# Optimization experiments

Hardware: AMD Instinct MI355X
Metric: run time of the kernel (lower is better)

Reference implementation:

```python
import jax, jax.numpy as jnp
import numpy as np

B, W, DIN, DOUT, H = 256, 20, 1024, 1024, 1280
EPS = 1e-5
SLOPE = 0.01  # torch LeakyReLU default negative_slope


def setup_inputs() -> dict:
    key = jax.random.key(0)
    ks = jax.random.split(key, 16)
    s = lambda fan_in: 1.0 / np.sqrt(fan_in)
    return {
        'embs': jax.random.normal(ks[0], (B, W, DIN), jnp.float32),
        'W1': jax.random.uniform(ks[1], (W, DIN, H), jnp.float32, -s(DIN), s(DIN)),
        'b1': jax.random.uniform(ks[2], (W, H), jnp.float32, -s(DIN), s(DIN)),
        'g1': jnp.ones((W, H), jnp.float32), 'bn1': jnp.zeros((W, H), jnp.float32),
        'W2': jax.random.uniform(ks[3], (W, H, H), jnp.float32, -s(H), s(H)),
        'b2': jax.random.uniform(ks[4], (W, H), jnp.float32, -s(H), s(H)),
        'g2': jnp.ones((W, H), jnp.float32), 'bn2': jnp.zeros((W, H), jnp.float32),
        'W3': jax.random.uniform(ks[5], (W, H, H), jnp.float32, -s(H), s(H)),
        'b3': jax.random.uniform(ks[6], (W, H), jnp.float32, -s(H), s(H)),
        'g3': jnp.ones((W, H), jnp.float32), 'bn3': jnp.zeros((W, H), jnp.float32),
        'W4': jax.random.uniform(ks[7], (W, H, DOUT), jnp.float32, -s(H), s(H)),
        'b4': jax.random.uniform(ks[8], (W, DOUT), jnp.float32, -s(H), s(H)),
    }


def _layernorm(x, g, b):
    # x: [B, W, H]; g, b: [W, H] (per-word affine params)
    mu = jnp.mean(x, axis=-1, keepdims=True)
    var = jnp.mean(jnp.square(x - mu), axis=-1, keepdims=True)
    return (x - mu) * jax.lax.rsqrt(var + EPS) * g + b


def _leaky_relu(x):
    return jnp.where(x >= 0, x, SLOPE * x)


def reference(embs, W1, b1, g1, bn1, W2, b2, g2, bn2, W3, b3, g3, bn3, W4, b4):
    # Stacked per-word towers: equivalent to the torch per-word Python loop.
    # embs: [B, W, DIN] -> out: [B, W, DOUT]
    h = jnp.einsum('bwi,wih->bwh', embs, W1) + b1
    h = _leaky_relu(_layernorm(h, g1, bn1))
    h = jnp.einsum('bwh,whk->bwk', h, W2) + b2
    h = _leaky_relu(_layernorm(h, g2, bn2))
    h = jnp.einsum('bwh,whk->bwk', h, W3) + b3
    h = _leaky_relu(_layernorm(h, g3, bn3))
    out = jnp.einsum('bwh,who->bwo', h, W4) + b4
    return out
```

## Files before the change

kernel.cpp:

```cpp
#include <hip/hip_runtime.h>
#include <hip/hip_bf16.h>


typedef unsigned short u16;
typedef __attribute__((ext_vector_type(8))) short bf16x8;
typedef __attribute__((ext_vector_type(4))) float f32x4;

constexpr int CB = 256;
constexpr int CW = 20;
constexpr int CDIN = 1024;
constexpr int CDOUT = 1024;
constexpr int CH = 1280;
constexpr float CEPS = 1e-5f;
constexpr float CSLOPE = 0.01f;

__device__ __forceinline__ u16 f2bf(float f) {
    union { float f; unsigned u; } v; v.f = f;
    unsigned r = v.u + 0x7fffu + ((v.u >> 16) & 1u);
    return (u16)(r >> 16);
}
__device__ __forceinline__ unsigned pk2(float a, float b) {
    return (unsigned)f2bf(a) | ((unsigned)f2bf(b) << 16);
}

template <int K, int N, bool AF32>
__global__ __launch_bounds__(256, 6) void gemm_kernel(
    const void* __restrict__ Aptr, const float* __restrict__ Bw,
    const float* __restrict__ bias, float* __restrict__ Out)
{
    constexpr int NB  = N / 64;
    constexpr int NK  = K / 32;
    constexpr int NWG = 4 * NB * CW;
    constexpr int CPX = NWG / 8;

    __shared__ u16 As[2][64 * 40];
    __shared__ u16 Bs[2][64 * 40];

    const int t   = threadIdx.x;
    const int bid = blockIdx.x;
    const int logical = (bid & 7) * CPX + (bid >> 3);
    const int mb = logical & 3;
    const int nb = (logical >> 2) % NB;
    const int w  = logical / (4 * NB);

    const int m0g = mb * 64;
    const int n0g = nb * 64;

    const int lane = t & 63;
    const int wid  = t >> 6;
    const int m0 = (wid >> 1) * 32;
    const int n0 = (wid & 1) * 32;
    const int lrow = lane & 15;
    const int kg   = lane >> 4;

    const int ar = t >> 2;
    const int ac = (t & 3) * 8;
    const u16*   agp  = (const u16*)Aptr   + ((size_t)(m0g + ar) * CW + w) * K + ac;
    const float* agpf = (const float*)Aptr + ((size_t)(m0g + ar) * CW + w) * K + ac;

    const int bn = t & 63;
    const int bq = t >> 6;
    const float* bgp = Bw + (size_t)w * K * N + (size_t)bq * 8 * N + (n0g + bn);

    f32x4 acc[2][2];
    #pragma unroll
    for (int i = 0; i < 2; ++i)
        #pragma unroll
        for (int j = 0; j < 2; ++j)
            acc[i][j] = (f32x4){0.f, 0.f, 0.f, 0.f};

    uint4 a0;
    float4 af0, af1;
    float bstg[8];

    auto loadA = [&](int k0) {
        if constexpr (AF32) {
            const float4* p = reinterpret_cast<const float4*>(agpf + k0);
            af0 = p[0]; af1 = p[1];
        } else {
            a0 = *reinterpret_cast<const uint4*>(agp + k0);
        }
    };
    auto loadB = [&](int k0) {
        const float* p = bgp + (size_t)k0 * N;
        #pragma unroll
        for (int i = 0; i < 8; ++i) bstg[i] = p[(size_t)i * N];
    };
    auto writeA = [&](int buf) {
        if constexpr (AF32) {
            uint4 pk;
            pk.x = pk2(af0.x, af0.y); pk.y = pk2(af0.z, af0.w);
            pk.z = pk2(af1.x, af1.y); pk.w = pk2(af1.z, af1.w);
            *reinterpret_cast<uint4*>(&As[buf][ar * 40 + ac]) = pk;
        } else {
            *reinterpret_cast<uint4*>(&As[buf][ar * 40 + ac]) = a0;
        }
    };
    auto writeB = [&](int buf) {
        uint4 pk;
        pk.x = pk2(bstg[0], bstg[1]); pk.y = pk2(bstg[2], bstg[3]);
        pk.z = pk2(bstg[4], bstg[5]); pk.w = pk2(bstg[6], bstg[7]);
        *reinterpret_cast<uint4*>(&Bs[buf][bn * 40 + bq * 8]) = pk;
    };
    auto compute = [&](int buf) {
        bf16x8 af[2], bfr[2];
        #pragma unroll
        for (int i = 0; i < 2; ++i)
            af[i] = *reinterpret_cast<const bf16x8*>(
                &As[buf][(m0 + i * 16 + lrow) * 40 + kg * 8]);
        #pragma unroll
        for (int j = 0; j < 2; ++j)
            bfr[j] = *reinterpret_cast<const bf16x8*>(
                &Bs[buf][(n0 + j * 16 + lrow) * 40 + kg * 8]);
        #pragma unroll
        for (int i = 0; i < 2; ++i)
            #pragma unroll
            for (int j = 0; j < 2; ++j)
                acc[i][j] = __builtin_amdgcn_mfma_f32_16x16x32_bf16(
                    af[i], bfr[j], acc[i][j], 0, 0, 0);
    };

    loadA(0); loadB(0);
    writeA(0); writeB(0);
    __syncthreads();

    int buf = 0;
    for (int ks = 0; ks < NK; ++ks) {
        if (ks + 1 < NK) { loadA((ks + 1) * 32); loadB((ks + 1) * 32); }
        compute(buf);
        if (ks + 1 < NK) { writeA(buf ^ 1); writeB(buf ^ 1); }
        __syncthreads();
        buf ^= 1;
    }

    const int rb = (lane >> 4) * 4;
    #pragma unroll
    for (int j = 0; j < 2; ++j) {
        const int gn = n0g + n0 + j * 16 + lrow;
        const float bv = bias[(size_t)w * N + gn];
        #pragma unroll
        for (int i = 0; i < 2; ++i) {
            const int gm = m0g + m0 + i * 16 + rb;
            #pragma unroll
            for (int r = 0; r < 4; ++r) {
                Out[((size_t)(gm + r) * CW + w) * N + gn] = acc[i][j][r] + bv;
            }
        }
    }
}

__global__ __launch_bounds__(320) void ln_lrelu_kernel(
    const float* __restrict__ h, const float* __restrict__ g,
    const float* __restrict__ bta, u16* __restrict__ out)
{
    const int row = blockIdx.x;
    const int w = row % CW;
    const int t = threadIdx.x;

    const float4 v = reinterpret_cast<const float4*>(h + (size_t)row * CH)[t];
    float s  = v.x + v.y + v.z + v.w;
    float sq = v.x * v.x + v.y * v.y + v.z * v.z + v.w * v.w;
    #pragma unroll
    for (int o = 32; o > 0; o >>= 1) {
        s  += __shfl_down(s, o, 64);
        sq += __shfl_down(sq, o, 64);
    }
    __shared__ float ss[5], sg[5];
    const int lane = t & 63, wv = t >> 6;
    if (lane == 0) { ss[wv] = s; sg[wv] = sq; }
    __syncthreads();
    float S = 0.f, Q = 0.f;
    #pragma unroll
    for (int i = 0; i < 5; ++i) { S += ss[i]; Q += sg[i]; }
    const float mean = S * (1.0f / CH);
    const float var  = Q * (1.0f / CH) - mean * mean;
    const float rstd = rsqrtf(var + CEPS);

    const float4 gg = reinterpret_cast<const float4*>(g   + (size_t)w * CH)[t];
    const float4 bb = reinterpret_cast<const float4*>(bta + (size_t)w * CH)[t];
    float4 y;
    y.x = (v.x - mean) * rstd * gg.x + bb.x;
    y.y = (v.y - mean) * rstd * gg.y + bb.y;
    y.z = (v.z - mean) * rstd * gg.z + bb.z;
    y.w = (v.w - mean) * rstd * gg.w + bb.w;
    y.x = y.x >= 0.f ? y.x : CSLOPE * y.x;
    y.y = y.y >= 0.f ? y.y : CSLOPE * y.y;
    y.z = y.z >= 0.f ? y.z : CSLOPE * y.z;
    y.w = y.w >= 0.f ? y.w : CSLOPE * y.w;
    ushort4 o4;
    o4.x = f2bf(y.x); o4.y = f2bf(y.y); o4.z = f2bf(y.z); o4.w = f2bf(y.w);
    reinterpret_cast<ushort4*>(out + (size_t)row * CH)[t] = o4;
}

extern "C" void kernel_launch(void* const* d_in, const int* in_sizes, int n_in,
                              void* d_out, int out_size, void* d_ws, size_t ws_size,
                              hipStream_t stream)
{
    const float* embs = (const float*)d_in[0];
    const float* W1  = (const float*)d_in[1];
    const float* b1  = (const float*)d_in[2];
    const float* g1  = (const float*)d_in[3];
    const float* bn1 = (const float*)d_in[4];
    const float* W2  = (const float*)d_in[5];
    const float* b2  = (const float*)d_in[6];
    const float* g2  = (const float*)d_in[7];
    const float* bn2 = (const float*)d_in[8];
    const float* W3  = (const float*)d_in[9];
    const float* b3  = (const float*)d_in[10];
    const float* g3  = (const float*)d_in[11];
    const float* bn3 = (const float*)d_in[12];
    const float* W4  = (const float*)d_in[13];
    const float* b4  = (const float*)d_in[14];

    char* ws = (char*)d_ws;
    float* h_raw = (float*)ws;
    u16*   a_bf  = (u16*)(ws + 26214400);

    gemm_kernel<CDIN, CH, true><<<4 * (CH / 64) * CW, 256, 0, stream>>>(embs, W1, b1, h_raw);
    ln_lrelu_kernel<<<CB * CW, 320, 0, stream>>>(h_raw, g1, bn1, a_bf);
    gemm_kernel<CH, CH, false><<<4 * (CH / 64) * CW, 256, 0, stream>>>(a_bf, W2, b2, h_raw);
    ln_lrelu_kernel<<<CB * CW, 320, 0, stream>>>(h_raw, g2, bn2, a_bf);
    gemm_kernel<CH, CH, false><<<4 * (CH / 64) * CW, 256, 0, stream>>>(a_bf, W3, b3, h_raw);
    ln_lrelu_kernel<<<CB * CW, 320, 0, stream>>>(h_raw, g3, bn3, a_bf);
    gemm_kernel<CH, CDOUT, false><<<4 * (CDOUT / 64) * CW, 256, 0, stream>>>(a_bf, W4, b4, (float*)d_out);
}
```

Measured before the change: 334.9 us.

## Double K tile to 64 with two-stage register prefetch in GEMM

The GEMM K step grows from 32 to 64 and global loads are prefetched two tiles ahead into two register staging slots. The loop is unrolled by two over the LDS double buffers. The fp32-to-bf16 packing now uses the HIP packed conversion intrinsic, and the occupancy hint drops to 4 to make room for the extra registers. This halves the number of barriers and hides more global latency, at the cost of more VGPRs and LDS per block and possibly lower occupancy.

Result: slower. 638.6 us (+90.7%).

```diff
diff --git a/kernel.cpp b/kernel.cpp
--- a/kernel.cpp
+++ b/kernel.cpp
@@ -20,21 +20,23 @@
     return (u16)(r >> 16);
 }
 __device__ __forceinline__ unsigned pk2(float a, float b) {
-    return (unsigned)f2bf(a) | ((unsigned)f2bf(b) << 16);
+    __hip_bfloat162 h = __float22bfloat162_rn(float2{a, b});
+    union { __hip_bfloat162 h; unsigned u; } v; v.h = h;
+    return v.u;
 }
 
 template <int K, int N, bool AF32>
-__global__ __launch_bounds__(256, 6) void gemm_kernel(
+__global__ __launch_bounds__(256, 4) void gemm_kernel(
     const void* __restrict__ Aptr, const float* __restrict__ Bw,
     const float* __restrict__ bias, float* __restrict__ Out)
 {
     constexpr int NB  = N / 64;
-    constexpr int NK  = K / 32;
+    constexpr int NK  = K / 64;
     constexpr int NWG = 4 * NB * CW;
     constexpr int CPX = NWG / 8;
 
-    __shared__ u16 As[2][64 * 40];
-    __shared__ u16 Bs[2][64 * 40];
+    __shared__ u16 As[2][64 * 72];
+    __shared__ u16 Bs[2][64 * 72];
 
     const int t   = threadIdx.x;
     const int bid = blockIdx.x;
@@ -54,13 +56,13 @@
     const int kg   = lane >> 4;
 
     const int ar = t >> 2;
-    const int ac = (t & 3) * 8;
+    const int ac = (t & 3) * 16;
     const u16*   agp  = (const u16*)Aptr   + ((size_t)(m0g + ar) * CW + w) * K + ac;
     const float* agpf = (const float*)Aptr + ((size_t)(m0g + ar) * CW + w) * K + ac;
 
     const int bn = t & 63;
     const int bq = t >> 6;
-    const float* bgp = Bw + (size_t)w * K * N + (size_t)bq * 8 * N + (n0g + bn);
+    const float* bgp = Bw + (size_t)w * K * N + (size_t)bq * 16 * N + (n0g + bn);
 
     f32x4 acc[2][2];
     #pragma unroll
@@ -69,68 +71,100 @@
         for (int j = 0; j < 2; ++j)
             acc[i][j] = (f32x4){0.f, 0.f, 0.f, 0.f};
 
-    uint4 a0;
-    float4 af0, af1;
-    float bstg[8];
-
-    auto loadA = [&](int k0) {
-        if constexpr (AF32) {
-            const float4* p = reinterpret_cast<const float4*>(agpf + k0);
-            af0 = p[0]; af1 = p[1];
-        } else {
-            a0 = *reinterpret_cast<const uint4*>(agp + k0);
+    uint4  a_s0[2], a_s1[2];
+    float4 af_s0[4], af_s1[4];
+    float  b_s0[16], b_s1[16];
+
+#define LOADA(k0, SL)                                                         \
+    do {                                                                      \
+        if constexpr (AF32) {                                                 \
+            const float4* p = reinterpret_cast<const float4*>(agpf + (k0));   \
+            af_s##SL[0] = p[0]; af_s##SL[1] = p[1];                           \
+            af_s##SL[2] = p[2]; af_s##SL[3] = p[3];                           \
+        } else {                                                              \
+            const uint4* p = reinterpret_cast<const uint4*>(agp + (k0));      \
+            a_s##SL[0] = p[0]; a_s##SL[1] = p[1];                             \
+        }                                                                     \
+    } while (0)
+
+#define LOADB(k0, SL)                                                         \
+    do {                                                                      \
+        const float* p = bgp + (size_t)(k0) * N;                              \
+        _Pragma("unroll")                                                     \
+        for (int i = 0; i < 16; ++i) b_s##SL[i] = p[(size_t)i * N];           \
+    } while (0)
+
+#define WRITEA(buf, SL)                                                       \
+    do {                                                                      \
+        if constexpr (AF32) {                                                 \
+            uint4 q0, q1;                                                     \
+            q0.x = pk2(af_s##SL[0].x, af_s##SL[0].y);                         \
+            q0.y = pk2(af_s##SL[0].z, af_s##SL[0].w);                         \
+            q0.z = pk2(af_s##SL[1].x, af_s##SL[1].y);                         \
+            q0.w = pk2(af_s##SL[1].z, af_s##SL[1].w);                         \
+            q1.x = pk2(af_s##SL[2].x, af_s##SL[2].y);                         \
+            q1.y = pk2(af_s##SL[2].z, af_s##SL[2].w);                         \
+            q1.z = pk2(af_s##SL[3].x, af_s##SL[3].y);                         \
+            q1.w = pk2(af_s##SL[3].z, af_s##SL[3].w);                         \
+            *reinterpret_cast<uint4*>(&As[buf][ar * 72 + ac])     = q0;       \
+            *reinterpret_cast<uint4*>(&As[buf][ar * 72 + ac + 8]) = q1;       \
+        } else {                                                              \
+            *reinterpret_cast<uint4*>(&As[buf][ar * 72 + ac])     = a_s##SL[0]; \
+            *reinterpret_cast<uint4*>(&As[buf][ar * 72 + ac + 8]) = a_s##SL[1]; \
+        }                                                                     \
+    } while (0)
+
+#define WRITEB(buf, SL)                                                       \
+    do {                                                                      \
+        uint4 q0, q1;                                                         \
+        q0.x = pk2(b_s##SL[0],  b_s##SL[1]);                                  \
+        q0.y = pk2(b_s##SL[2],  b_s##SL[3]);                                  \
+        q0.z = pk2(b_s##SL[4],  b_s##SL[5]);                                  \
+        q0.w = pk2(b_s##SL[6],  b_s##SL[7]);                                  \
+        q1.x = pk2(b_s##SL[8],  b_s##SL[9]);                                  \
+        q1.y = pk2(b_s##SL[10], b_s##SL[11]);                                 \
+        q1.z = pk2(b_s##SL[12], b_s##SL[13]);                                 \
+        q1.w = pk2(b_s##SL[14], b_s##SL[15]);                                 \
+        *reinterpret_cast<uint4*>(&Bs[buf][bn * 72 + bq * 16])     = q0;      \
+        *reinterpret_cast<uint4*>(&Bs[buf][bn * 72 + bq * 16 + 8]) = q1;      \
+    } while (0)
+
+    auto compute = [&](int buf) {
+        #pragma unroll
+        for (int kc = 0; kc < 2; ++kc) {
+            bf16x8 af[2], bf[2];
+            #pragma unroll
+            for (int i = 0; i < 2; ++i)
+                af[i] = *reinterpret_cast<const bf16x8*>(
+                    &As[buf][(m0 + i * 16 + lrow) * 72 + kc * 32 + kg * 8]);
+            #pragma unroll
+            for (int j = 0; j < 2; ++j)
+                bf[j] = *reinterpret_cast<const bf16x8*>(
+                    &Bs[buf][(n0 + j * 16 + lrow) * 72 + kc * 32 + kg * 8]);
+            #pragma unroll
+            for (int i = 0; i < 2; ++i)
+                #pragma unroll
+                for (int j = 0; j < 2; ++j)
+                    acc[i][j] = __builtin_amdgcn_mfma_f32_16x16x32_bf16(
+                        af[i], bf[j], acc[i][j], 0, 0, 0);
         }
     };
-    auto loadB = [&](int k0) {
-        const float* p = bgp + (size_t)k0 * N;
-        #pragma unroll
-        for (int i = 0; i < 8; ++i) bstg[i] = p[(size_t)i * N];
-    };
-    auto writeA = [&](int buf) {
-        if constexpr (AF32) {
-            uint4 pk;
-            pk.x = pk2(af0.x, af0.y); pk.y = pk2(af0.z, af0.w);
-            pk.z = pk2(af1.x, af1.y); pk.w = pk2(af1.z, af1.w);
-            *reinterpret_cast<uint4*>(&As[buf][ar * 40 + ac]) = pk;
-        } else {
-            *reinterpret_cast<uint4*>(&As[buf][ar * 40 + ac]) = a0;
-        }
-    };
-    auto writeB = [&](int buf) {
-        uint4 pk;
-        pk.x = pk2(bstg[0], bstg[1]); pk.y = pk2(bstg[2], bstg[3]);
-        pk.z = pk2(bstg[4], bstg[5]); pk.w = pk2(bstg[6], bstg[7]);
-        *reinterpret_cast<uint4*>(&Bs[buf][bn * 40 + bq * 8]) = pk;
-    };
-    auto compute = [&](int buf) {
-        bf16x8 af[2], bfr[2];
-        #pragma unroll
-        for (int i = 0; i < 2; ++i)
-            af[i] = *reinterpret_cast<const bf16x8*>(
-                &As[buf][(m0 + i * 16 + lrow) * 40 + kg * 8]);
-        #pragma unroll
-        for (int j = 0; j < 2; ++j)
-            bfr[j] = *reinterpret_cast<const bf16x8*>(
-                &Bs[buf][(n0 + j * 16 + lrow) * 40 + kg * 8]);
-        #pragma unroll
-        for (int i = 0; i < 2; ++i)
-            #pragma unroll
-            for (int j = 0; j < 2; ++j)
-                acc[i][j] = __builtin_amdgcn_mfma_f32_16x16x32_bf16(
-                    af[i], bfr[j], acc[i][j], 0, 0, 0);
-    };
-
-    loadA(0); loadB(0);
-    writeA(0); writeB(0);
+
+    LOADA(0, 0); LOADB(0, 0);
+    LOADA(64, 1); LOADB(64, 1);
+    WRITEA(0, 0); WRITEB(0, 0);
     __syncthreads();
 
-    int buf = 0;
-    for (int ks = 0; ks < NK; ++ks) {
-        if (ks + 1 < NK) { loadA((ks + 1) * 32); loadB((ks + 1) * 32); }
-        compute(buf);
-        if (ks + 1 < NK) { writeA(buf ^ 1); writeB(buf ^ 1); }
+    for (int ks = 0; ks < NK; ks += 2) {
+        if (ks + 2 < NK) { LOADA((ks + 2) * 64, 0); LOADB((ks + 2) * 64, 0); }
+        compute(0);
+        if (ks + 1 < NK) { WRITEA(1, 1); WRITEB(1, 1); }
         __syncthreads();
-        buf ^= 1;
+
+        if (ks + 3 < NK) { LOADA((ks + 3) * 64, 1); LOADB((ks + 3) * 64, 1); }
+        compute(1);
+        if (ks + 2 < NK) { WRITEA(0, 0); WRITEB(0, 0); }
+        __syncthreads();
     }
 
     const int rb = (lane >> 4) * 4;
@@ -147,6 +181,10 @@
             }
         }
     }
+#undef LOADA
+#undef LOADB
+#undef WRITEA
+#undef WRITEB
 }
 
 __global__ __launch_bounds__(320) void ln_lrelu_kernel(
```
